# Kernel tuning notes

Hardware: AMD Instinct MI355X
Metric: run time of the kernel (lower is better)

Reference implementation:

```python
import jax, jax.numpy as jnp
import numpy as np

HEADS, HEAD_DIM = 8, 32
FOLD_W = FOLD_H = 8
PW = PH = 2  # proposal_w/h -> M = PW*PH centers per region


def setup_inputs() -> dict:
    key = jax.random.key(0)
    ks = jax.random.split(key, 8)
    dim, hd = 96, HEADS * HEAD_DIM
    return {
        "x": jax.random.normal(ks[0], (16, dim, 64, 64), jnp.float32),
        "Wf": jax.random.normal(ks[1], (hd, dim), jnp.float32) * 0.05,
        "bf": jax.random.normal(ks[2], (hd,), jnp.float32) * 0.01,
        "Wv": jax.random.normal(ks[3], (hd, dim), jnp.float32) * 0.05,
        "bv": jax.random.normal(ks[4], (hd,), jnp.float32) * 0.01,
        "Wp": jax.random.normal(ks[5], (dim, hd), jnp.float32) * 0.05,
        "bp": jax.random.normal(ks[6], (dim,), jnp.float32) * 0.01,
        "sim_alpha": jnp.ones((1,), jnp.float32),
        "sim_beta": jnp.zeros((1,), jnp.float32),
    }


def _l2norm(t):
    # matches torch F.normalize(dim=-1, eps=1e-12)
    n = jnp.maximum(jnp.linalg.norm(t, axis=-1, keepdims=True), 1e-12)
    return t / n


def _cluster_forward(x, Wf, bf, Wv, bv, Wp, bp, sim_alpha, sim_beta):
    B, C, W, H = x.shape
    # 1x1 convs
    v = jnp.einsum("bchw,oc->bohw", x, Wv) + bv[None, :, None, None]
    f = jnp.einsum("bchw,oc->bohw", x, Wf) + bf[None, :, None, None]

    def split_heads(t):  # b (e c) w h -> (b e) c w h
        b = t.shape[0]
        return t.reshape(b, HEADS, HEAD_DIM, W, H).reshape(b * HEADS, HEAD_DIM, W, H)

    f, v = split_heads(f), split_heads(v)

    def fold(t):  # b c (f1 w) (f2 h) -> (b f1 f2) c w h
        b, c, w0, h0 = t.shape
        ws, hs = w0 // FOLD_W, h0 // FOLD_H
        t = t.reshape(b, c, FOLD_W, ws, FOLD_H, hs)
        return t.transpose(0, 2, 4, 1, 3, 5).reshape(b * FOLD_W * FOLD_H, c, ws, hs)

    f, v = fold(f), fold(v)
    b, c, w, h = f.shape

    def pool(t):  # AdaptiveMaxPool2d((PW,PH)); divides evenly -> block max
        return t.reshape(b, c, PW, w // PW, PH, h // PH).max(axis=(3, 5))

    centers = pool(f).reshape(b, c, PW * PH).transpose(0, 2, 1)       # [b,M,c]
    value_centers = pool(v).reshape(b, c, PW * PH).transpose(0, 2, 1)  # [b,M,c]
    pts = f.reshape(b, c, w * h).transpose(0, 2, 1)                    # [b,N,c]

    cos = jnp.einsum("bmc,bnc->bmn", _l2norm(centers), _l2norm(pts))
    sim = jax.nn.sigmoid(sim_beta + sim_alpha * cos)                   # [b,M,N]

    # hard assignment: each point keeps only its best center
    idx = jnp.argmax(sim, axis=1)                                      # [b,N]
    mask = jax.nn.one_hot(idx, sim.shape[1], dtype=sim.dtype)          # [b,N,M]
    mask = jnp.transpose(mask, (0, 2, 1))                              # [b,M,N]
    sim = sim * mask

    value2 = v.reshape(b, c, w * h).transpose(0, 2, 1)                 # [b,N,c]
    # gather points -> centers
    agg = (jnp.einsum("bnc,bmn->bmc", value2, sim) + value_centers) / (
        mask.sum(axis=-1, keepdims=True) + 1.0
    )
    # dispatch centers -> points
    out = jnp.einsum("bmc,bmn->bnc", agg, sim)                         # [b,N,c]
    out = out.transpose(0, 2, 1).reshape(b, c, w, h)

    # unfold regions back
    bb = b // (FOLD_W * FOLD_H)
    out = out.reshape(bb, FOLD_W, FOLD_H, c, w, h).transpose(0, 3, 1, 4, 2, 5)
    out = out.reshape(bb, c, FOLD_W * w, FOLD_H * h)
    # merge heads: (b e) c w h -> b (e c) w h
    out = out.reshape(bb // HEADS, HEADS * HEAD_DIM, W, H)
    out = jnp.einsum("bchw,oc->bohw", out, Wp) + bp[None, :, None, None]
    return out


def reference(x, Wf, bf, Wv, bv, Wp, bp, sim_alpha, sim_beta):
    return _cluster_forward(x, Wf, bf, Wv, bv, Wp, bp, sim_alpha, sim_beta)
```

## Files before the change

### kernel.cpp

```cpp
#include <hip/hip_runtime.h>
#include <math.h>


#define TPB 256

__global__ __launch_bounds__(TPB, 5)
void cc_main(const float* __restrict__ x,
             const float* __restrict__ Wf, const float* __restrict__ bf,
             const float* __restrict__ Wv, const float* __restrict__ bv,
             const float* __restrict__ Wp,
             const float* __restrict__ salpha, const float* __restrict__ sbeta,
             float* __restrict__ cd)
{
    __shared__ __align__(16) float smem[6144];
    __shared__ float cfs[2][132], cvs[2][132], swb[2][256], aggs[2][132];
    __shared__ float2 bib[2][64];
    __shared__ float cnts[2][4];

    const int t    = threadIdx.x;
    const int lane = t & 63;
    const int wid  = __builtin_amdgcn_readfirstlane(t >> 6);
    const int tc   = t >> 4;
    const int tp   = t & 15;
    const int blk  = blockIdx.x;
    const int f1   = blk & 7;
    const int f2   = (blk >> 3) & 7;
    const int heg  = (blk >> 6) & 3;
    const int bb   = blk >> 8;
    const int fold = f1*8 + f2;

    const float* xb = x + (size_t)bb*96*4096 + (size_t)(f1*8)*64 + f2*8;

    float acc[8][4];
    {
        const float* bsrc = (tc < 8) ? (bf + heg*64 + tc*8)
                                     : (bv + heg*64 + (tc-8)*8);
        float4 b0 = *(const float4*)bsrc;
        float4 b1 = *(const float4*)(bsrc + 4);
        #pragma unroll
        for (int i = 0; i < 4; ++i) {
            acc[0][i]=b0.x; acc[1][i]=b0.y; acc[2][i]=b0.z; acc[3][i]=b0.w;
            acc[4][i]=b1.x; acc[5][i]=b1.y; acc[6][i]=b1.z; acc[7][i]=b1.w;
        }
    }

    int xoff[2], xdst[2];
    #pragma unroll
    for (int i = 0; i < 2; ++i) {
        int fl = i*256 + t;
        int kl = fl >> 4, sg = fl & 15;
        xoff[i] = kl*4096 + (sg >> 1)*64 + (sg & 1)*4;
        xdst[i] = 4096 + kl*64 + sg*4;
    }
    int wdst[4];
    const float* wptr[4];
    #pragma unroll
    for (int i = 0; i < 4; ++i) {
        int fl = i*256 + t;
        int rr = fl & 127, kq = fl >> 7;
        wptr[i] = ((rr < 64) ? (Wf + (size_t)(heg*64 + rr)*96)
                             : (Wv + (size_t)(heg*64 + rr - 64)*96)) + kq*4;
        wdst[i] = (kq*4)*128 + rr;
    }

    float4 pxr[2], pwr[4];
    #pragma unroll
    for (int i = 0; i < 2; ++i) pxr[i] = *(const float4*)(xb + xoff[i]);
    #pragma unroll
    for (int i = 0; i < 4; ++i) pwr[i] = *(const float4*)(wptr[i]);
    #pragma unroll
    for (int i = 0; i < 2; ++i) *(float4*)&smem[xdst[i]] = pxr[i];
    #pragma unroll
    for (int i = 0; i < 4; ++i) {
        smem[wdst[i]      ] = pwr[i].x;
        smem[wdst[i] + 128] = pwr[i].y;
        smem[wdst[i] + 256] = pwr[i].z;
        smem[wdst[i] + 384] = pwr[i].w;
    }
    __syncthreads();

    for (int kc = 0; ; ) {
        if (kc < 64) {
            #pragma unroll
            for (int i = 0; i < 2; ++i)
                pxr[i] = *(const float4*)(xb + (kc+32)*4096 + xoff[i]);
            #pragma unroll
            for (int i = 0; i < 4; ++i)
                pwr[i] = *(const float4*)(wptr[i] + kc + 32);
        }
        #pragma unroll 4
        for (int k = 0; k < 32; ++k) {
            float4 wa  = *(const float4*)&smem[k*128 + tc*8];
            float4 wb4 = *(const float4*)&smem[k*128 + tc*8 + 4];
            float4 xq  = *(const float4*)&smem[4096 + k*64 + tp*4];
            float xv[4] = {xq.x, xq.y, xq.z, xq.w};
            #pragma unroll
            for (int i = 0; i < 4; ++i) {
                acc[0][i] = fmaf(wa.x,  xv[i], acc[0][i]);
                acc[1][i] = fmaf(wa.y,  xv[i], acc[1][i]);
                acc[2][i] = fmaf(wa.z,  xv[i], acc[2][i]);
                acc[3][i] = fmaf(wa.w,  xv[i], acc[3][i]);
                acc[4][i] = fmaf(wb4.x, xv[i], acc[4][i]);
                acc[5][i] = fmaf(wb4.y, xv[i], acc[5][i]);
                acc[6][i] = fmaf(wb4.z, xv[i], acc[6][i]);
                acc[7][i] = fmaf(wb4.w, xv[i], acc[7][i]);
            }
        }
        if (kc == 64) break;
        __syncthreads();
        #pragma unroll
        for (int i = 0; i < 2; ++i) *(float4*)&smem[xdst[i]] = pxr[i];
        #pragma unroll
        for (int i = 0; i < 4; ++i) {
            smem[wdst[i]      ] = pwr[i].x;
            smem[wdst[i] + 128] = pwr[i].y;
            smem[wdst[i] + 256] = pwr[i].z;
            smem[wdst[i] + 384] = pwr[i].w;
        }
        __syncthreads();
        kc += 32;
    }

    const float alpha = salpha[0], beta = sbeta[0];
    __syncthreads();

    if (wid < 2) {
        #pragma unroll
        for (int j = 0; j < 8; ++j)
            #pragma unroll
            for (int i2 = 0; i2 < 4; ++i2)
                smem[(tc*8 + j)*65 + tp*4 + i2] = acc[j][i2];
    } else {
        const int he = wid - 2;
        const int m  = ((tp >> 3) << 1) | (tp & 1);
        const int c0 = ((tc - 8) & 3) * 8;
        #pragma unroll
        for (int j = 0; j < 8; ++j) {
            float mv = fmaxf(fmaxf(acc[j][0], acc[j][1]),
                             fmaxf(acc[j][2], acc[j][3]));
            mv = fmaxf(mv, __shfl_xor(mv, 2));
            mv = fmaxf(mv, __shfl_xor(mv, 4));
            if ((tp & 6) == 0) cvs[he][m*33 + c0 + j] = mv;
        }
    }
    __syncthreads();

    if (wid < 2) {
        const int he = wid, slot = he;
        {
            int m = lane >> 4, c0 = (lane & 15)*2;
            int pw = m >> 1, ph = m & 1;
            #pragma unroll
            for (int cc = 0; cc < 2; ++cc) {
                int c = c0 + cc;
                float mf = -3.402823466e38f;
                #pragma unroll
                for (int a = 0; a < 4; ++a)
                    #pragma unroll
                    for (int b2 = 0; b2 < 4; ++b2) {
                        int n = (pw*4 + a)*8 + ph*4 + b2;
                        mf = fmaxf(mf, smem[(he*32 + c)*65 + n]);
                    }
                cfs[slot][m*33 + c] = mf;
            }
        }
        float d0=0,d1=0,d2=0,d3=0,pn=0,cn0=0,cn1=0,cn2=0,cn3=0;
        #pragma unroll 8
        for (int c = 0; c < 32; ++c) {
            float fv = smem[(he*32 + c)*65 + lane];
            float m0 = cfs[slot][c], m1 = cfs[slot][33+c];
            float m2 = cfs[slot][66+c], m3 = cfs[slot][99+c];
            d0 = fmaf(m0, fv, d0); d1 = fmaf(m1, fv, d1);
            d2 = fmaf(m2, fv, d2); d3 = fmaf(m3, fv, d3);
            pn = fmaf(fv, fv, pn);
            cn0 = fmaf(m0, m0, cn0); cn1 = fmaf(m1, m1, cn1);
            cn2 = fmaf(m2, m2, cn2); cn3 = fmaf(m3, m3, cn3);
        }
        float ip = 1.f / fmaxf(sqrtf(pn), 1e-12f);
        float z0 = beta + alpha*(d0*(1.f/fmaxf(sqrtf(cn0),1e-12f))*ip);
        float z1 = beta + alpha*(d1*(1.f/fmaxf(sqrtf(cn1),1e-12f))*ip);
        float z2 = beta + alpha*(d2*(1.f/fmaxf(sqrtf(cn2),1e-12f))*ip);
        float z3 = beta + alpha*(d3*(1.f/fmaxf(sqrtf(cn3),1e-12f))*ip);
        float s0 = 1.f/(1.f + expf(-z0));
        float s1 = 1.f/(1.f + expf(-z1));
        float s2 = 1.f/(1.f + expf(-z2));
        float s3 = 1.f/(1.f + expf(-z3));
        int bi = 0; float bvv = s0;
        if (s1 > bvv) { bvv = s1; bi = 1; }
        if (s2 > bvv) { bvv = s2; bi = 2; }
        if (s3 > bvv) { bvv = s3; bi = 3; }
        int cnt0 = __popcll(__ballot(bi == 0));
        int cnt1 = __popcll(__ballot(bi == 1));
        int cnt2 = __popcll(__ballot(bi == 2));
        int cnt3 = __popcll(__ballot(bi == 3));
        swb[slot][lane]       = (bi==0) ? bvv : 0.f;
        swb[slot][64 + lane]  = (bi==1) ? bvv : 0.f;
        swb[slot][128 + lane] = (bi==2) ? bvv : 0.f;
        swb[slot][192 + lane] = (bi==3) ? bvv : 0.f;
        bib[slot][lane] = make_float2(bvv, (float)bi);
        if (lane == 0) {
            cnts[slot][0] = (float)cnt0; cnts[slot][1] = (float)cnt1;
            cnts[slot][2] = (float)cnt2; cnts[slot][3] = (float)cnt3;
        }
    }
    __syncthreads();

    float* tb = cd + ((size_t)(bb*64 + fold))*4096;

    if (wid >= 2) {
        const int he = wid - 2, slot = he;
        const int c0 = ((tc - 8) & 3) * 8;
        float s[8][4];
        #pragma unroll
        for (int j = 0; j < 8; ++j)
            #pragma unroll
            for (int m = 0; m < 4; ++m) s[j][m] = 0.f;
        #pragma unroll
        for (int i = 0; i < 4; ++i) {
            int n = tp*4 + i;
            float w0 = swb[slot][n],       w1 = swb[slot][64 + n];
            float w2 = swb[slot][128 + n], w3 = swb[slot][192 + n];
            #pragma unroll
            for (int j = 0; j < 8; ++j) {
                float v = acc[j][i];
                s[j][0] = fmaf(v, w0, s[j][0]);
                s[j][1] = fmaf(v, w1, s[j][1]);
                s[j][2] = fmaf(v, w2, s[j][2]);
                s[j][3] = fmaf(v, w3, s[j][3]);
            }
        }
        #pragma unroll
        for (int j = 0; j < 8; ++j)
            #pragma unroll
            for (int m = 0; m < 4; ++m) {
                float v = s[j][m];
                v += __shfl_xor(v, 1);
                v += __shfl_xor(v, 2);
                v += __shfl_xor(v, 4);
                v += __shfl_xor(v, 8);
                s[j][m] = v;
            }
        if (tp == 0) {
            #pragma unroll
            for (int m = 0; m < 4; ++m) {
                float inv = 1.f;
                #pragma unroll
                for (int j = 0; j < 8; ++j)
                    aggs[slot][m*33 + c0 + j] =
                        (s[j][m] + cvs[slot][m*33 + c0 + j])
                        / (cnts[slot][m] + 1.f);
                (void)inv;
            }
        }
        float2 b2 = bib[slot][lane];
        *(float2*)&tb[3072 + (heg*2 + he)*128 + lane*2] = b2;
    }
    __syncthreads();

    #pragma unroll
    for (int it = 0; it < 3; ++it) {
        int idx = it*256 + t;
        int he  = (idx >= 384) ? 1 : 0;
        int rem = idx - he*384;
        int oc  = rem >> 2, m = rem & 3;
        const float* wp = Wp + (size_t)oc*256 + heg*64 + he*32;
        const float* ag = aggs[he] + m*33;
        float s = 0.f;
        #pragma unroll
        for (int c = 0; c < 32; ++c)
            s = fmaf(wp[c], ag[c], s);
        tb[(heg*2 + he)*384 + oc*4 + m] = s;
    }
}

__global__ __launch_bounds__(TPB, 8)
void cc_comb(const float* __restrict__ cd, const float* __restrict__ bp,
             float* __restrict__ out)
{
    __shared__ __align__(16) float ld[4096];
    const int t    = threadIdx.x;
    const int lane = t & 63;
    const int wid  = __builtin_amdgcn_readfirstlane(t >> 6);
    const int blk  = blockIdx.x;
    const int f1   = blk & 7;
    const int f2   = (blk >> 3) & 7;
    const int bb   = blk >> 6;
    const float* tb = cd + ((size_t)(bb*64 + f1*8 + f2))*4096;

    #pragma unroll
    for (int i = 0; i < 4; ++i) {
        float4 v = *(const float4*)(tb + (t*4 + i)*4);
        *(float4*)&ld[(t*4 + i)*4] = v;
    }
    __syncthreads();

    const int oc0 = wid*24;
    float acc[24];
    #pragma unroll
    for (int j = 0; j < 24; j += 4) {
        float4 b = *(const float4*)(bp + oc0 + j);
        acc[j]=b.x; acc[j+1]=b.y; acc[j+2]=b.z; acc[j+3]=b.w;
    }

    #pragma unroll
    for (int he = 0; he < 8; ++he) {
        float2 sv = *(const float2*)&ld[3072 + he*128 + lane*2];
        const int bi = (int)sv.y;
        const float s0 = (bi==0) ? sv.x : 0.f;
        const float s1 = (bi==1) ? sv.x : 0.f;
        const float s2 = (bi==2) ? sv.x : 0.f;
        const float s3 = (bi==3) ? sv.x : 0.f;
        const float* pr = &ld[he*384 + oc0*4];
        #pragma unroll
        for (int j = 0; j < 24; ++j) {
            float4 p = *(const float4*)(pr + j*4);
            acc[j] = fmaf(p.x, s0, acc[j]);
            acc[j] = fmaf(p.y, s1, acc[j]);
            acc[j] = fmaf(p.z, s2, acc[j]);
            acc[j] = fmaf(p.w, s3, acc[j]);
        }
    }

    const int r = lane >> 3, hh = lane & 7;
    const size_t ob = (size_t)bb*96*4096 + (size_t)(f1*8 + r)*64 + f2*8 + hh;
    #pragma unroll
    for (int j = 0; j < 24; ++j)
        out[ob + (size_t)(oc0 + j)*4096] = acc[j];
}

extern "C" void kernel_launch(void* const* d_in, const int* in_sizes, int n_in,
                              void* d_out, int out_size, void* d_ws, size_t ws_size,
                              hipStream_t stream) {
    (void)in_sizes; (void)n_in; (void)out_size; (void)ws_size;
    float* cd = (float*)d_ws;
    cc_main<<<dim3(4096), dim3(TPB), 0, stream>>>(
        (const float*)d_in[0],
        (const float*)d_in[1],
        (const float*)d_in[2],
        (const float*)d_in[3],
        (const float*)d_in[4],
        (const float*)d_in[5],
        (const float*)d_in[7],
        (const float*)d_in[8],
        cd);
    cc_comb<<<dim3(1024), dim3(TPB), 0, stream>>>(
        cd,
        (const float*)d_in[6],
        (float*)d_out);
}
```

Measured before the change: 214.5 us.

## Process two adjacent folds per block sharing staged weight tiles

Doubles the block to 512 threads so each block handles two horizontally adjacent fold regions. The Wf/Wv weight chunk staged in shared memory is then shared by both halves, which halves weight global loads and staging work per fold and halves the grid size. The per-point assignment weights are rebuilt from the best-index pair instead of a separate swb buffer, and cfa is reused for the aggregates to save LDS. Costs are a larger LDS footprint, larger blocks that may reduce scheduling flexibility, and a launch-bounds request of 8 that may force register spills.

```diff
diff --git a/kernel.cpp b/kernel.cpp
--- a/kernel.cpp
+++ b/kernel.cpp
@@ -2,9 +2,9 @@
 #include <math.h>
 
 
-#define TPB 256
-
-__global__ __launch_bounds__(TPB, 5)
+#define TPB 512
+
+__global__ __launch_bounds__(TPB, 8)
 void cc_main(const float* __restrict__ x,
              const float* __restrict__ Wf, const float* __restrict__ bf,
              const float* __restrict__ Wv, const float* __restrict__ bv,
@@ -12,29 +12,31 @@
              const float* __restrict__ salpha, const float* __restrict__ sbeta,
              float* __restrict__ cd)
 {
-    __shared__ __align__(16) float smem[6144];
-    __shared__ float cfs[2][132], cvs[2][132], swb[2][256], aggs[2][132];
-    __shared__ float2 bib[2][64];
-    __shared__ float cnts[2][4];
+    __shared__ __align__(16) float smem[8320];
+    __shared__ float cvs[2][2][132];
+    __shared__ float cfa[2][2][132];
+    __shared__ float2 bib[2][2][64];
+    __shared__ float cnts[2][2][4];
 
     const int t    = threadIdx.x;
     const int lane = t & 63;
     const int wid  = __builtin_amdgcn_readfirstlane(t >> 6);
-    const int tc   = t >> 4;
-    const int tp   = t & 15;
+    const int fh   = wid >> 2;
+    const int wl   = wid & 3;
+    const int th   = t & 255;
+    const int tc   = th >> 4;
+    const int tp   = th & 15;
     const int blk  = blockIdx.x;
     const int f1   = blk & 7;
-    const int f2   = (blk >> 3) & 7;
-    const int heg  = (blk >> 6) & 3;
-    const int bb   = blk >> 8;
-    const int fold = f1*8 + f2;
-
-    const float* xb = x + (size_t)bb*96*4096 + (size_t)(f1*8)*64 + f2*8;
+    const int f2p  = (blk >> 3) & 3;
+    const int heg  = (blk >> 5) & 3;
+    const int bb   = blk >> 7;
+
+    const float* xb = x + (size_t)bb*96*4096 + (size_t)(f1*8)*64 + f2p*16;
 
     float acc[8][4];
     {
-        const float* bsrc = (tc < 8) ? (bf + heg*64 + tc*8)
-                                     : (bv + heg*64 + (tc-8)*8);
+        const float* bsrc = ((tc < 8) ? bf : bv) + heg*64 + (tc & 7)*8;
         float4 b0 = *(const float4*)bsrc;
         float4 b1 = *(const float4*)(bsrc + 4);
         #pragma unroll
@@ -47,31 +49,31 @@
     int xoff[2], xdst[2];
     #pragma unroll
     for (int i = 0; i < 2; ++i) {
-        int fl = i*256 + t;
-        int kl = fl >> 4, sg = fl & 15;
-        xoff[i] = kl*4096 + (sg >> 1)*64 + (sg & 1)*4;
-        xdst[i] = 4096 + kl*64 + sg*4;
-    }
-    int wdst[4];
-    const float* wptr[4];
-    #pragma unroll
-    for (int i = 0; i < 4; ++i) {
-        int fl = i*256 + t;
+        int fl = i*512 + t;
+        int kl = fl >> 5, p4 = (fl & 31)*4;
+        xoff[i] = kl*4096 + ((p4 >> 3) & 7)*64 + (p4 >> 6)*8 + (p4 & 7);
+        xdst[i] = 4096 + kl*128 + p4;
+    }
+    int wdst[2];
+    const float* wptr[2];
+    #pragma unroll
+    for (int i = 0; i < 2; ++i) {
+        int fl = i*512 + t;
         int rr = fl & 127, kq = fl >> 7;
         wptr[i] = ((rr < 64) ? (Wf + (size_t)(heg*64 + rr)*96)
                              : (Wv + (size_t)(heg*64 + rr - 64)*96)) + kq*4;
         wdst[i] = (kq*4)*128 + rr;
     }
 
-    float4 pxr[2], pwr[4];
+    float4 pxr[2], pwr[2];
     #pragma unroll
     for (int i = 0; i < 2; ++i) pxr[i] = *(const float4*)(xb + xoff[i]);
     #pragma unroll
-    for (int i = 0; i < 4; ++i) pwr[i] = *(const float4*)(wptr[i]);
+    for (int i = 0; i < 2; ++i) pwr[i] = *(const float4*)(wptr[i]);
     #pragma unroll
     for (int i = 0; i < 2; ++i) *(float4*)&smem[xdst[i]] = pxr[i];
     #pragma unroll
-    for (int i = 0; i < 4; ++i) {
+    for (int i = 0; i < 2; ++i) {
         smem[wdst[i]      ] = pwr[i].x;
         smem[wdst[i] + 128] = pwr[i].y;
         smem[wdst[i] + 256] = pwr[i].z;
@@ -85,14 +87,14 @@
             for (int i = 0; i < 2; ++i)
                 pxr[i] = *(const float4*)(xb + (kc+32)*4096 + xoff[i]);
             #pragma unroll
-            for (int i = 0; i < 4; ++i)
+            for (int i = 0; i < 2; ++i)
                 pwr[i] = *(const float4*)(wptr[i] + kc + 32);
         }
         #pragma unroll 4
         for (int k = 0; k < 32; ++k) {
             float4 wa  = *(const float4*)&smem[k*128 + tc*8];
             float4 wb4 = *(const float4*)&smem[k*128 + tc*8 + 4];
-            float4 xq  = *(const float4*)&smem[4096 + k*64 + tp*4];
+            float4 xq  = *(const float4*)&smem[4096 + k*128 + fh*64 + tp*4];
             float xv[4] = {xq.x, xq.y, xq.z, xq.w};
             #pragma unroll
             for (int i = 0; i < 4; ++i) {
@@ -111,7 +113,7 @@
         #pragma unroll
         for (int i = 0; i < 2; ++i) *(float4*)&smem[xdst[i]] = pxr[i];
         #pragma unroll
-        for (int i = 0; i < 4; ++i) {
+        for (int i = 0; i < 2; ++i) {
             smem[wdst[i]      ] = pwr[i].x;
             smem[wdst[i] + 128] = pwr[i].y;
             smem[wdst[i] + 256] = pwr[i].z;
@@ -122,16 +124,19 @@
     }
 
     const float alpha = salpha[0], beta = sbeta[0];
-    __syncthreads();
-
-    if (wid < 2) {
+    const int fold = f1*8 + f2p*2 + fh;
+    float* tb = cd + ((size_t)(bb*64 + fold))*4096;
+    float* fd = &smem[fh*4160];
+    __syncthreads();
+
+    if (wl < 2) {
         #pragma unroll
         for (int j = 0; j < 8; ++j)
             #pragma unroll
             for (int i2 = 0; i2 < 4; ++i2)
-                smem[(tc*8 + j)*65 + tp*4 + i2] = acc[j][i2];
+                fd[(tc*8 + j)*65 + tp*4 + i2] = acc[j][i2];
     } else {
-        const int he = wid - 2;
+        const int he = wl - 2;
         const int m  = ((tp >> 3) << 1) | (tp & 1);
         const int c0 = ((tc - 8) & 3) * 8;
         #pragma unroll
@@ -140,13 +145,13 @@
                              fmaxf(acc[j][2], acc[j][3]));
             mv = fmaxf(mv, __shfl_xor(mv, 2));
             mv = fmaxf(mv, __shfl_xor(mv, 4));
-            if ((tp & 6) == 0) cvs[he][m*33 + c0 + j] = mv;
-        }
-    }
-    __syncthreads();
-
-    if (wid < 2) {
-        const int he = wid, slot = he;
+            if ((tp & 6) == 0) cvs[fh][he][m*33 + c0 + j] = mv;
+        }
+    }
+    __syncthreads();
+
+    if (wl < 2) {
+        const int he = wl;
         {
             int m = lane >> 4, c0 = (lane & 15)*2;
             int pw = m >> 1, ph = m & 1;
@@ -159,17 +164,17 @@
                     #pragma unroll
                     for (int b2 = 0; b2 < 4; ++b2) {
                         int n = (pw*4 + a)*8 + ph*4 + b2;
-                        mf = fmaxf(mf, smem[(he*32 + c)*65 + n]);
+                        mf = fmaxf(mf, fd[(he*32 + c)*65 + n]);
                     }
-                cfs[slot][m*33 + c] = mf;
+                cfa[fh][he][m*33 + c] = mf;
             }
         }
         float d0=0,d1=0,d2=0,d3=0,pn=0,cn0=0,cn1=0,cn2=0,cn3=0;
         #pragma unroll 8
         for (int c = 0; c < 32; ++c) {
-            float fv = smem[(he*32 + c)*65 + lane];
-            float m0 = cfs[slot][c], m1 = cfs[slot][33+c];
-            float m2 = cfs[slot][66+c], m3 = cfs[slot][99+c];
+            float fv = fd[(he*32 + c)*65 + lane];
+            float m0 = cfa[fh][he][c], m1 = cfa[fh][he][33+c];
+            float m2 = cfa[fh][he][66+c], m3 = cfa[fh][he][99+c];
             d0 = fmaf(m0, fv, d0); d1 = fmaf(m1, fv, d1);
             d2 = fmaf(m2, fv, d2); d3 = fmaf(m3, fv, d3);
             pn = fmaf(fv, fv, pn);
@@ -193,22 +198,16 @@
         int cnt1 = __popcll(__ballot(bi == 1));
         int cnt2 = __popcll(__ballot(bi == 2));
         int cnt3 = __popcll(__ballot(bi == 3));
-        swb[slot][lane]       = (bi==0) ? bvv : 0.f;
-        swb[slot][64 + lane]  = (bi==1) ? bvv : 0.f;
-        swb[slot][128 + lane] = (bi==2) ? bvv : 0.f;
-        swb[slot][192 + lane] = (bi==3) ? bvv : 0.f;
-        bib[slot][lane] = make_float2(bvv, (float)bi);
+        bib[fh][he][lane] = make_float2(bvv, (float)bi);
         if (lane == 0) {
-            cnts[slot][0] = (float)cnt0; cnts[slot][1] = (float)cnt1;
-            cnts[slot][2] = (float)cnt2; cnts[slot][3] = (float)cnt3;
-        }
-    }
-    __syncthreads();
-
-    float* tb = cd + ((size_t)(bb*64 + fold))*4096;
-
-    if (wid >= 2) {
-        const int he = wid - 2, slot = he;
+            cnts[fh][he][0] = (float)cnt0; cnts[fh][he][1] = (float)cnt1;
+            cnts[fh][he][2] = (float)cnt2; cnts[fh][he][3] = (float)cnt3;
+        }
+    }
+    __syncthreads();
+
+    if (wl >= 2) {
+        const int he = wl - 2;
         const int c0 = ((tc - 8) & 3) * 8;
         float s[8][4];
         #pragma unroll
@@ -218,8 +217,12 @@
         #pragma unroll
         for (int i = 0; i < 4; ++i) {
             int n = tp*4 + i;
-            float w0 = swb[slot][n],       w1 = swb[slot][64 + n];
-            float w2 = swb[slot][128 + n], w3 = swb[slot][192 + n];
+            float2 b2 = bib[fh][he][n];
+            int bi = (int)b2.y;
+            float w0 = (bi==0) ? b2.x : 0.f;
+            float w1 = (bi==1) ? b2.x : 0.f;
+            float w2 = (bi==2) ? b2.x : 0.f;
+            float w3 = (bi==3) ? b2.x : 0.f;
             #pragma unroll
             for (int j = 0; j < 8; ++j) {
                 float v = acc[j][i];
@@ -242,38 +245,38 @@
             }
         if (tp == 0) {
             #pragma unroll
-            for (int m = 0; m < 4; ++m) {
-                float inv = 1.f;
+            for (int m = 0; m < 4; ++m)
                 #pragma unroll
                 for (int j = 0; j < 8; ++j)
-                    aggs[slot][m*33 + c0 + j] =
-                        (s[j][m] + cvs[slot][m*33 + c0 + j])
-                        / (cnts[slot][m] + 1.f);
-                (void)inv;
-            }
-        }
-        float2 b2 = bib[slot][lane];
+                    cfa[fh][he][m*33 + c0 + j] =
+                        (s[j][m] + cvs[fh][he][m*33 + c0 + j])
+                        / (cnts[fh][he][m] + 1.f);
+        }
+        float2 b2 = bib[fh][he][lane];
         *(float2*)&tb[3072 + (heg*2 + he)*128 + lane*2] = b2;
     }
     __syncthreads();
 
     #pragma unroll
     for (int it = 0; it < 3; ++it) {
-        int idx = it*256 + t;
-        int he  = (idx >= 384) ? 1 : 0;
-        int rem = idx - he*384;
-        int oc  = rem >> 2, m = rem & 3;
+        int idx = it*512 + t;
+        int fp  = (idx >= 768) ? 1 : 0;
+        int rem = idx - fp*768;
+        int he  = (rem >= 384) ? 1 : 0;
+        int rem2 = rem - he*384;
+        int oc  = rem2 >> 2, m = rem2 & 3;
         const float* wp = Wp + (size_t)oc*256 + heg*64 + he*32;
-        const float* ag = aggs[he] + m*33;
+        const float* ag = &cfa[fp][he][m*33];
         float s = 0.f;
         #pragma unroll
         for (int c = 0; c < 32; ++c)
             s = fmaf(wp[c], ag[c], s);
-        tb[(heg*2 + he)*384 + oc*4 + m] = s;
+        const int foldp = f1*8 + f2p*2 + fp;
+        cd[((size_t)(bb*64 + foldp))*4096 + (heg*2 + he)*384 + oc*4 + m] = s;
     }
 }
 
-__global__ __launch_bounds__(TPB, 8)
+__global__ __launch_bounds__(256, 8)
 void cc_comb(const float* __restrict__ cd, const float* __restrict__ bp,
              float* __restrict__ out)
 {
@@ -333,7 +336,7 @@
                               hipStream_t stream) {
     (void)in_sizes; (void)n_in; (void)out_size; (void)ws_size;
     float* cd = (float*)d_ws;
-    cc_main<<<dim3(4096), dim3(TPB), 0, stream>>>(
+    cc_main<<<dim3(2048), dim3(TPB), 0, stream>>>(
         (const float*)d_in[0],
         (const float*)d_in[1],
         (const float*)d_in[2],
@@ -343,7 +346,7 @@
         (const float*)d_in[7],
         (const float*)d_in[8],
         cd);
-    cc_comb<<<dim3(1024), dim3(TPB), 0, stream>>>(
+    cc_comb<<<dim3(1024), dim3(256), 0, stream>>>(
         cd,
         (const float*)d_in[6],
         (float*)d_out);
```

Result: slower. 256.6 us (+19.6%).
